# Kernel tuning notes

Hardware: AMD Instinct MI355X
Metric: run time of the kernel (lower is better)

The kernel has to match this reference:

```python
import jax, jax.numpy as jnp
import numpy as np

EPSILON = 0.1
ALPHA = 0.5
N_ITER = 10
N_USERS = 100000


def setup_inputs() -> dict:
    key = jax.random.key(0)
    k1, k2, k3, k4, k5, k6 = jax.random.split(key, 6)
    B, C, F = 2048, 1024, 128
    users = jax.random.randint(k1, (B,), 0, N_USERS)
    items = jax.random.randint(k2, (B, C), 0, C)
    D = jax.random.uniform(k3, (B, C), minval=0.1, maxval=1.0)
    capacities = jax.random.uniform(k4, (C,), minval=0.5, maxval=1.5)
    # ScaledEmbedding: normal init scaled down by embedding_dim
    item_emb = jax.random.normal(k5, (C, F), dtype=jnp.float32) / F
    user_emb = jax.random.normal(k6, (N_USERS, F), dtype=jnp.float32) / F
    return dict(users=users, items=items, D=D, capacities=capacities,
                item_emb=item_emb, user_emb=user_emb)


def reference(users, items, D, capacities, item_emb, user_emb):
    B, C = D.shape
    ie = item_emb[items]            # [B, C, F] gathered candidate embeddings
    ue = user_emb[users]            # [B, F]
    dot = jnp.einsum('bcf,bf->bc', ie, ue)          # batched dot products
    affinity = (1.0 - ALPHA) * dot - ALPHA * (D / jnp.mean(D))
    K = jnp.exp(affinity / EPSILON)                 # [B, C]

    scaling = B / N_USERS
    a = jnp.ones((B,), K.dtype)
    b = capacities * scaling                        # [C]

    def step(carry, _):
        _, v = carry
        u = a / (K @ v)                             # [B]
        v_new = b / (K.T @ u)                       # [C]
        return (u, v_new), None

    (u, v), _ = jax.lax.scan(step, (a, jnp.ones((C,), K.dtype)),
                             None, length=N_ITER)
    P = K * (u[:, None] * v[None, :])               # K * outer(u, v)
    return P
```

## Files before the change

### kernel.cpp

```cpp
#include <hip/hip_runtime.h>
#include <hip/hip_fp16.h>

#define BB      2048
#define CC      1024
#define FF      128
#define NBLK    256
#define RPB     8
#define TPB     512
#define NITER   10
#define SUBR    8
#define SCALING_F (2048.0f / 100000.0f)

__device__ float g_K[BB * CC];
__device__ float g_meanPart[NBLK];
__device__ float g_colsum[NITER * SUBR * CC];

__global__ void __launch_bounds__(TPB)
k0_prep(const float* __restrict__ D) {
    const int bid = blockIdx.x, tid = threadIdx.x;
    for (int i = bid * TPB + tid; i < NITER * SUBR * CC; i += NBLK * TPB)
        g_colsum[i] = 0.0f;
    const float4* D4 = (const float4*)D;
    float p = 0.0f;
    for (int i = bid * TPB + tid; i < BB * CC / 4; i += NBLK * TPB) {
        float4 d = D4[i];
        p += d.x + d.y + d.z + d.w;
    }
    #pragma unroll
    for (int off = 32; off > 0; off >>= 1) p += __shfl_down(p, off, 64);
    __shared__ float red[TPB / 64];
    if ((tid & 63) == 0) red[tid >> 6] = p;
    __syncthreads();
    if (tid == 0) {
        float s = 0.0f;
        #pragma unroll
        for (int k = 0; k < TPB / 64; ++k) s += red[k];
        g_meanPart[bid] = s;
    }
}

__global__ void __launch_bounds__(TPB)
k1_buildK(const int* __restrict__ users, const int* __restrict__ items,
          const float* __restrict__ D, const float* __restrict__ iemb,
          const float* __restrict__ uemb) {
    const int bid = blockIdx.x, tid = threadIdx.x;
    const int r0 = bid * RPB;

    __shared__ float  uesh[RPB][FF];
    __shared__ __half dott[RPB][CC];
    __shared__ float  s2sh;

    if (tid < 256) {
        int r = tid >> 5, f4 = tid & 31;
        int u = users[r0 + r];
        ((float4*)uesh[r])[f4] = ((const float4*)(uemb + (size_t)u * FF))[f4];
    }
    if (tid < 64) {
        float s = g_meanPart[tid] + g_meanPart[tid + 64] +
                  g_meanPart[tid + 128] + g_meanPart[tid + 192];
        #pragma unroll
        for (int off = 32; off > 0; off >>= 1) s += __shfl_down(s, off, 64);
        if (tid == 0) s2sh = 5.0f * (float)(BB * CC) / s;
    }
    __syncthreads();

    const float4* us = (const float4*)uesh;
    #pragma unroll
    for (int jj = 0; jj < CC / TPB; ++jj) {
        int j = jj * TPB + tid;
        float acc[RPB] = {};
        const float4* ip = (const float4*)(iemb + (size_t)j * FF);
        for (int f4 = 0; f4 < FF / 4; ++f4) {
            float4 a = ip[f4];
            #pragma unroll
            for (int r = 0; r < RPB; ++r) {
                float4 b = us[r * (FF / 4) + f4];
                acc[r] += a.x * b.x + a.y * b.y + a.z * b.z + a.w * b.w;
            }
        }
        #pragma unroll
        for (int r = 0; r < RPB; ++r) dott[r][j] = __float2half(acc[r]);
    }
    __syncthreads();

    const float s2 = s2sh;
    const int4*   it4 = (const int4*)(items + ((size_t)r0 << 10));
    const float4* D4  = (const float4*)(D + ((size_t)r0 << 10));
    float4*       K4  = (float4*)(g_K + ((size_t)r0 << 10));
    for (int i = tid; i < RPB * CC / 4; i += TPB) {
        int4 iv = it4[i];
        float4 d = D4[i];
        int r = i >> 8;
        float4 kv;
        kv.x = __expf(5.0f * __half2float(dott[r][iv.x]) - s2 * d.x);
        kv.y = __expf(5.0f * __half2float(dott[r][iv.y]) - s2 * d.y);
        kv.z = __expf(5.0f * __half2float(dott[r][iv.z]) - s2 * d.z);
        kv.w = __expf(5.0f * __half2float(dott[r][iv.w]) - s2 * d.w);
        K4[i] = kv;
    }
}

__global__ void __launch_bounds__(TPB)
k_iter(const float* __restrict__ caps, int t) {
    const int bid = blockIdx.x, tid = threadIdx.x;
    const int r0 = bid * RPB;

    __shared__ float Kt[RPB][CC];
    __shared__ float vsh[CC];
    __shared__ float ush[RPB];

    for (int c = tid; c < CC; c += TPB) {
        float v = 1.0f;
        if (t > 0) {
            const float* base = g_colsum + (size_t)(t - 1) * SUBR * CC;
            float s = 0.0f;
            #pragma unroll
            for (int k = 0; k < SUBR; ++k) s += base[k * CC + c];
            v = caps[c] * SCALING_F / s;
        }
        vsh[c] = v;
    }
    const float4* Kg = (const float4*)(g_K + ((size_t)r0 << 10));
    float4* KtL = (float4*)Kt;
    for (int i = tid; i < RPB * CC / 4; i += TPB) KtL[i] = Kg[i];
    __syncthreads();

    {
        int r = tid >> 6, l = tid & 63;
        const float4* kr = (const float4*)Kt[r];
        const float4* v4 = (const float4*)vsh;
        float p = 0.0f;
        #pragma unroll
        for (int i = 0; i < 4; ++i) {
            float4 k = kr[l + i * 64], v = v4[l + i * 64];
            p += k.x * v.x + k.y * v.y + k.z * v.z + k.w * v.w;
        }
        #pragma unroll
        for (int off = 32; off > 0; off >>= 1) p += __shfl_down(p, off, 64);
        if (l == 0) ush[r] = 1.0f / p;
    }
    __syncthreads();

    float* cb = g_colsum + ((size_t)t * SUBR + (bid & (SUBR - 1))) * CC;
    for (int c = tid; c < CC; c += TPB) {
        float s = 0.0f;
        #pragma unroll
        for (int r = 0; r < RPB; ++r) s += Kt[r][c] * ush[r];
        atomicAdd(&cb[c], s);
    }
}

__global__ void __launch_bounds__(TPB)
k_final(const float* __restrict__ caps, float* __restrict__ out) {
    const int bid = blockIdx.x, tid = threadIdx.x;
    const int r0 = bid * RPB;

    __shared__ float Kt[RPB][CC];
    __shared__ float vsh[CC];
    __shared__ float ush[RPB];

    for (int c = tid; c < CC; c += TPB) {
        const float* base = g_colsum + (size_t)(NITER - 2) * SUBR * CC;
        float s = 0.0f;
        #pragma unroll
        for (int k = 0; k < SUBR; ++k) s += base[k * CC + c];
        vsh[c] = caps[c] * SCALING_F / s;
    }
    const float4* Kg = (const float4*)(g_K + ((size_t)r0 << 10));
    float4* KtL = (float4*)Kt;
    for (int i = tid; i < RPB * CC / 4; i += TPB) KtL[i] = Kg[i];
    __syncthreads();

    {
        int r = tid >> 6, l = tid & 63;
        const float4* kr = (const float4*)Kt[r];
        const float4* v4 = (const float4*)vsh;
        float p = 0.0f;
        #pragma unroll
        for (int i = 0; i < 4; ++i) {
            float4 k = kr[l + i * 64], v = v4[l + i * 64];
            p += k.x * v.x + k.y * v.y + k.z * v.z + k.w * v.w;
        }
        #pragma unroll
        for (int off = 32; off > 0; off >>= 1) p += __shfl_down(p, off, 64);
        if (l == 0) ush[r] = 1.0f / p;
    }
    __syncthreads();

    for (int c = tid; c < CC; c += TPB) {
        const float* base = g_colsum + (size_t)(NITER - 1) * SUBR * CC;
        float s = 0.0f;
        #pragma unroll
        for (int k = 0; k < SUBR; ++k) s += base[k * CC + c];
        vsh[c] = caps[c] * SCALING_F / s;
    }
    __syncthreads();

    float4* o4 = (float4*)(out + ((size_t)r0 << 10));
    for (int i = tid; i < RPB * CC / 4; i += TPB) {
        int r = i >> 8;
        float4 k = KtL[i];
        float  ur = ush[r];
        float4 v = *(const float4*)&vsh[(i * 4) & (CC - 1)];
        float4 p;
        p.x = k.x * ur * v.x;  p.y = k.y * ur * v.y;
        p.z = k.z * ur * v.z;  p.w = k.w * ur * v.w;
        o4[i] = p;
    }
}

extern "C" void kernel_launch(void* const* d_in, const int* in_sizes, int n_in,
                              void* d_out, int out_size, void* d_ws, size_t ws_size,
                              hipStream_t stream) {
    const int*   users = (const int*)d_in[0];
    const int*   items = (const int*)d_in[1];
    const float* D     = (const float*)d_in[2];
    const float* caps  = (const float*)d_in[3];
    const float* iemb  = (const float*)d_in[4];
    const float* uemb  = (const float*)d_in[5];
    float* out = (float*)d_out;

    hipLaunchKernelGGL(k0_prep,   dim3(NBLK), dim3(TPB), 0, stream, D);
    hipLaunchKernelGGL(k1_buildK, dim3(NBLK), dim3(TPB), 0, stream,
                       users, items, D, iemb, uemb);
    for (int t = 0; t < NITER; ++t)
        hipLaunchKernelGGL(k_iter, dim3(NBLK), dim3(TPB), 0, stream, caps, t);
    hipLaunchKernelGGL(k_final,  dim3(NBLK), dim3(TPB), 0, stream, caps, out);
}
```

Before: 192.6 us.

## Store Sinkhorn kernel matrix K in fp16 and read it directly from global

The exponentiated affinity matrix K is now written as packed half2 values instead of fp32, halving its footprint and the bytes read by each of the ten iteration kernels and the final kernel. The LDS staging copy of each block's K rows is removed. Row dot products and column sums now read K straight from global memory, so each block reads its rows twice and relies on cache hits for the second pass. This trades fp16 rounding of K, which bounds accuracy of the scaling vectors and the output, for lower memory traffic and less shared memory per block.

```diff
diff --git a/kernel.cpp b/kernel.cpp
--- a/kernel.cpp
+++ b/kernel.cpp
@@ -11,7 +11,7 @@
 #define SUBR    8
 #define SCALING_F (2048.0f / 100000.0f)
 
-__device__ float g_K[BB * CC];
+__device__ __align__(16) __half g_Kh[BB * CC];
 __device__ float g_meanPart[NBLK];
 __device__ float g_colsum[NITER * SUBR * CC];
 
@@ -86,7 +86,7 @@
     const float s2 = s2sh;
     const int4*   it4 = (const int4*)(items + ((size_t)r0 << 10));
     const float4* D4  = (const float4*)(D + ((size_t)r0 << 10));
-    float4*       K4  = (float4*)(g_K + ((size_t)r0 << 10));
+    uint2* K2 = (uint2*)(g_Kh + ((size_t)r0 << 10));
     for (int i = tid; i < RPB * CC / 4; i += TPB) {
         int4 iv = it4[i];
         float4 d = D4[i];
@@ -96,7 +96,12 @@
         kv.y = __expf(5.0f * __half2float(dott[r][iv.y]) - s2 * d.y);
         kv.z = __expf(5.0f * __half2float(dott[r][iv.z]) - s2 * d.z);
         kv.w = __expf(5.0f * __half2float(dott[r][iv.w]) - s2 * d.w);
-        K4[i] = kv;
+        __half2 lo = __floats2half2_rn(kv.x, kv.y);
+        __half2 hi = __floats2half2_rn(kv.z, kv.w);
+        uint2 o;
+        o.x = *reinterpret_cast<unsigned*>(&lo);
+        o.y = *reinterpret_cast<unsigned*>(&hi);
+        K2[i] = o;
     }
 }
 
@@ -105,7 +110,6 @@
     const int bid = blockIdx.x, tid = threadIdx.x;
     const int r0 = bid * RPB;
 
-    __shared__ float Kt[RPB][CC];
     __shared__ float vsh[CC];
     __shared__ float ush[RPB];
 
@@ -120,33 +124,39 @@
         }
         vsh[c] = v;
     }
-    const float4* Kg = (const float4*)(g_K + ((size_t)r0 << 10));
-    float4* KtL = (float4*)Kt;
-    for (int i = tid; i < RPB * CC / 4; i += TPB) KtL[i] = Kg[i];
-    __syncthreads();
-
-    {
-        int r = tid >> 6, l = tid & 63;
-        const float4* kr = (const float4*)Kt[r];
-        const float4* v4 = (const float4*)vsh;
+    __syncthreads();
+
+    {
+        int w = tid >> 6, l = tid & 63;
+        const __half2* kr = (const __half2*)(g_Kh + ((size_t)(r0 + w) << 10));
+        const float2*  v2 = (const float2*)vsh;
         float p = 0.0f;
         #pragma unroll
-        for (int i = 0; i < 4; ++i) {
-            float4 k = kr[l + i * 64], v = v4[l + i * 64];
-            p += k.x * v.x + k.y * v.y + k.z * v.z + k.w * v.w;
-        }
-        #pragma unroll
-        for (int off = 32; off > 0; off >>= 1) p += __shfl_down(p, off, 64);
-        if (l == 0) ush[r] = 1.0f / p;
-    }
-    __syncthreads();
-
-    float* cb = g_colsum + ((size_t)t * SUBR + (bid & (SUBR - 1))) * CC;
-    for (int c = tid; c < CC; c += TPB) {
-        float s = 0.0f;
-        #pragma unroll
-        for (int r = 0; r < RPB; ++r) s += Kt[r][c] * ush[r];
-        atomicAdd(&cb[c], s);
+        for (int i = 0; i < 8; ++i) {
+            float2 k = __half22float2(kr[l + 64 * i]);
+            float2 v = v2[l + 64 * i];
+            p += k.x * v.x + k.y * v.y;
+        }
+        #pragma unroll
+        for (int off = 32; off > 0; off >>= 1) p += __shfl_xor(p, off, 64);
+        if (l == 0) ush[w] = 1.0f / p;
+    }
+    __syncthreads();
+
+    {
+        float sx = 0.0f, sy = 0.0f;
+        #pragma unroll
+        for (int r = 0; r < RPB; ++r) {
+            const __half2* kp =
+                (const __half2*)(g_Kh + ((size_t)(r0 + r) << 10)) + tid;
+            float2 k = __half22float2(*kp);
+            float ur = ush[r];
+            sx += k.x * ur; sy += k.y * ur;
+        }
+        float* cb = g_colsum + ((size_t)t * SUBR + (bid & (SUBR - 1))) * CC
+                  + 2 * tid;
+        atomicAdd(cb, sx);
+        atomicAdd(cb + 1, sy);
     }
 }
 
@@ -155,7 +165,6 @@
     const int bid = blockIdx.x, tid = threadIdx.x;
     const int r0 = bid * RPB;
 
-    __shared__ float Kt[RPB][CC];
     __shared__ float vsh[CC];
     __shared__ float ush[RPB];
 
@@ -166,24 +175,22 @@
         for (int k = 0; k < SUBR; ++k) s += base[k * CC + c];
         vsh[c] = caps[c] * SCALING_F / s;
     }
-    const float4* Kg = (const float4*)(g_K + ((size_t)r0 << 10));
-    float4* KtL = (float4*)Kt;
-    for (int i = tid; i < RPB * CC / 4; i += TPB) KtL[i] = Kg[i];
-    __syncthreads();
-
-    {
-        int r = tid >> 6, l = tid & 63;
-        const float4* kr = (const float4*)Kt[r];
-        const float4* v4 = (const float4*)vsh;
+    __syncthreads();
+
+    {
+        int w = tid >> 6, l = tid & 63;
+        const __half2* kr = (const __half2*)(g_Kh + ((size_t)(r0 + w) << 10));
+        const float2*  v2 = (const float2*)vsh;
         float p = 0.0f;
         #pragma unroll
-        for (int i = 0; i < 4; ++i) {
-            float4 k = kr[l + i * 64], v = v4[l + i * 64];
-            p += k.x * v.x + k.y * v.y + k.z * v.z + k.w * v.w;
-        }
-        #pragma unroll
-        for (int off = 32; off > 0; off >>= 1) p += __shfl_down(p, off, 64);
-        if (l == 0) ush[r] = 1.0f / p;
+        for (int i = 0; i < 8; ++i) {
+            float2 k = __half22float2(kr[l + 64 * i]);
+            float2 v = v2[l + 64 * i];
+            p += k.x * v.x + k.y * v.y;
+        }
+        #pragma unroll
+        for (int off = 32; off > 0; off >>= 1) p += __shfl_xor(p, off, 64);
+        if (l == 0) ush[w] = 1.0f / p;
     }
     __syncthreads();
 
@@ -196,16 +203,17 @@
     }
     __syncthreads();
 
-    float4* o4 = (float4*)(out + ((size_t)r0 << 10));
-    for (int i = tid; i < RPB * CC / 4; i += TPB) {
-        int r = i >> 8;
-        float4 k = KtL[i];
-        float  ur = ush[r];
-        float4 v = *(const float4*)&vsh[(i * 4) & (CC - 1)];
-        float4 p;
-        p.x = k.x * ur * v.x;  p.y = k.y * ur * v.y;
-        p.z = k.z * ur * v.z;  p.w = k.w * ur * v.w;
-        o4[i] = p;
+    {
+        float2 v = *(const float2*)&vsh[2 * tid];
+        #pragma unroll
+        for (int r = 0; r < RPB; ++r) {
+            const __half2* kp =
+                (const __half2*)(g_Kh + ((size_t)(r0 + r) << 10)) + tid;
+            float2 k = __half22float2(*kp);
+            float ur = ush[r];
+            float2 p; p.x = k.x * ur * v.x; p.y = k.y * ur * v.y;
+            ((float2*)(out + ((size_t)(r0 + r) << 10)))[tid] = p;
+        }
     }
 }
 
```

Result: slower. 204.6 us (+6.3%).
